# Kernel tuning notes

Measured on AMD Instinct MI355X. Metric: run time of the kernel, lower is better.

Reference implementation:

```python
import jax, jax.numpy as jnp
import numpy as np

# Hardcoded output spatial dims from the original call() (EEG: 62 channels x 375 timesteps)
H, W = 62, 375
N = 16            # batch size
P = H * W         # 23250 patch positions (x_1 dim of cal_val)
KFLAT = 1 * 5 * 25  # flattened kernel size = prod(output_dimension)
F = 64            # number of filters


def setup_inputs() -> dict:
    key = jax.random.key(0)
    k1, k2, k3 = jax.random.split(key, 3)
    x = jax.random.normal(k1, (N, P, KFLAT), dtype=jnp.float32)            # cal_val
    encoding_vector = jax.random.normal(k2, (P, KFLAT), dtype=jnp.float32)
    w = jax.random.normal(k3, (1, 5, 25, F), dtype=jnp.float32) * 0.05      # learned kernel
    return {"x": x, "encoding_vector": encoding_vector, "w": w}


def reference(x, encoding_vector, w):
    n, p, k = x.shape
    f = w.shape[-1]
    # build() flattens each filter: Kernel[j] = w[:, :, :, j].reshape(-1)  -> [F, kflat]
    kernel = jnp.moveaxis(w, 3, 0).reshape(f, k)
    # Original per-filter loop computes sum_k (kernel[f,k] + enc[p,k]) * x[n,p,k]
    # without materializing the tiled [N, P, kflat] kernel tensor:
    # out[f,n,p] = <kernel[f], x[n,p]> + <enc[p], x[n,p]>
    out_fnp = jnp.einsum('fk,npk->fnp', kernel, x) \
        + jnp.einsum('pk,npk->np', encoding_vector, x)[None, :, :]
    # Faithful final reshape of stacked [F, N, P] tensor into [N, F, H, W]
    return out_fnp.reshape(n, f, H, W)
```

## Files before the change

### kernel.cpp

```cpp
#include <hip/hip_runtime.h>


#define P_    23250u
#define K_    125
#define F_    64
#define M_TOT 372000
#define BM    128
#define LDROW 256
#define NBLK  ((M_TOT + BM - 1) / BM)

typedef __bf16 bf16;
typedef __bf16 bf16x4 __attribute__((ext_vector_type(4)));
typedef __bf16 bf16x8 __attribute__((ext_vector_type(8)));
typedef float  f32x4  __attribute__((ext_vector_type(4)));
typedef float  f32x4u __attribute__((ext_vector_type(4), aligned(4)));

__global__ __launch_bounds__(256, 1)
void prep_wfrag(const float* __restrict__ w, bf16* __restrict__ wfrag)
{
    const int tid = threadIdx.x;
    const int f  = ((tid >> 6) << 4) | (tid & 15);
    const int kg = (tid >> 4) & 3;
    #pragma unroll
    for (int ks = 0; ks < 4; ++ks) {
        bf16x8 fr;
        #pragma unroll
        for (int j = 0; j < 8; ++j) {
            const int k = ks * 32 + kg * 8 + j;
            fr[j] = (bf16)((k < K_) ? w[k * F_ + f] : 0.0f);
        }
        *(bf16x8*)(wfrag + tid * 32 + ks * 8) = fr;
    }
}

template<bool USE_WS>
__global__ __launch_bounds__(256, 4)
void eegconv_kernel(const float* __restrict__ x,
                    const float* __restrict__ enc,
                    const float* __restrict__ w,
                    const bf16* __restrict__ wfrag,
                    float* __restrict__ out)
{
    __shared__ bf16  xt[BM * 128];
    __shared__ float srow[BM];

    const int tid  = threadIdx.x;
    const int lane = tid & 63;
    const int wv   = tid >> 6;
    const int fl   = lane & 15;
    const int kg   = lane >> 4;
    const int r0   = blockIdx.x * BM;

    bf16x8 kf[4];
    if (USE_WS) {
        const bf16x8* wf = (const bf16x8*)(wfrag + tid * 32);
        #pragma unroll
        for (int ks = 0; ks < 4; ++ks) kf[ks] = wf[ks];
    } else {
        const int f = wv * 16 + fl;
        #pragma unroll
        for (int ks = 0; ks < 4; ++ks)
            #pragma unroll
            for (int j = 0; j < 8; ++j) {
                const int k = ks * 32 + kg * 8 + j;
                kf[ks][j] = (bf16)((k < K_) ? w[k * F_ + f] : 0.0f);
            }
    }

    {
        const int row = tid >> 1;
        const int t2  = tid & 1;
        int gi = r0 + row;
        const bool rv = gi < M_TOT;
        if (!rv) gi = 0;
        const float* xr = x   + (size_t)gi * K_;
        const float* er = enc + (size_t)((unsigned)gi % P_) * K_;
        char* lbase = (char*)xt + row * LDROW;
        const int sw = (row & 7) << 4;
        float part = 0.0f;

        #pragma unroll
        for (int u = 0; u < 15; ++u) {
            const int c = u * 2 + t2;
            const f32x4 xv = (f32x4)*(const f32x4u*)(xr + c * 4);
            const f32x4 ev = (f32x4)*(const f32x4u*)(er + c * 4);
            part += ev.x * xv.x + ev.y * xv.y + ev.z * xv.z + ev.w * xv.w;
            bf16x4 bv;
            bv[0] = (bf16)xv.x; bv[1] = (bf16)xv.y; bv[2] = (bf16)xv.z; bv[3] = (bf16)xv.w;
            *(bf16x4*)(lbase + ((c * 8) ^ sw)) = bv;
        }
        {
            const int c = 30 + t2;
            f32x4 xv, ev;
            if (t2 == 0) {
                xv = (f32x4)*(const f32x4u*)(xr + 120);
                ev = (f32x4)*(const f32x4u*)(er + 120);
            } else {
                xv = f32x4{xr[124], 0.f, 0.f, 0.f};
                ev = f32x4{er[124], 0.f, 0.f, 0.f};
            }
            part += ev.x * xv.x + ev.y * xv.y + ev.z * xv.z + ev.w * xv.w;
            bf16x4 bv;
            bv[0] = (bf16)xv.x; bv[1] = (bf16)xv.y; bv[2] = (bf16)xv.z; bv[3] = (bf16)xv.w;
            *(bf16x4*)(lbase + ((c * 8) ^ sw)) = bv;
        }
        part += __shfl_xor(part, 1);
        if (t2 == 0) srow[row] = part;
    }
    __syncthreads();

    f32x4 acc[8];
    #pragma unroll
    for (int t = 0; t < 8; ++t) acc[t] = f32x4{0.f, 0.f, 0.f, 0.f};

    #pragma unroll
    for (int t = 0; t < 8; ++t) {
        const int il = t * 16 + fl;
        const char* rbase = (const char*)xt + il * LDROW;
        const int sw = (il & 7) << 4;
        #pragma unroll
        for (int ks = 0; ks < 4; ++ks) {
            const bf16x8 av = *(const bf16x8*)(rbase + ((ks * 64 + kg * 16) ^ sw));
            acc[t] = __builtin_amdgcn_mfma_f32_16x16x32_bf16(av, kf[ks], acc[t], 0, 0, 0);
        }
    }

    const size_t fM = (size_t)(wv * 16 + fl) * (size_t)M_TOT;
    #pragma unroll
    for (int t = 0; t < 8; ++t) {
        const int ib = t * 16 + kg * 4;
        const int i0 = r0 + ib;
        if (i0 < M_TOT) {
            const f32x4 sv = *(const f32x4*)&srow[ib];
            f32x4 v;
            v.x = acc[t][0] + sv.x;
            v.y = acc[t][1] + sv.y;
            v.z = acc[t][2] + sv.z;
            v.w = acc[t][3] + sv.w;
            *(f32x4*)(out + fM + i0) = v;
        }
    }
}

extern "C" void kernel_launch(void* const* d_in, const int* in_sizes, int n_in,
                              void* d_out, int out_size, void* d_ws, size_t ws_size,
                              hipStream_t stream)
{
    const float* x   = (const float*)d_in[0];
    const float* enc = (const float*)d_in[1];
    const float* w   = (const float*)d_in[2];
    float* out = (float*)d_out;

    if (ws_size >= 16384) {
        bf16* wfrag = (bf16*)d_ws;
        prep_wfrag<<<1, 256, 0, stream>>>(w, wfrag);
        eegconv_kernel<true><<<NBLK, 256, 0, stream>>>(x, enc, w, wfrag, out);
    } else {
        eegconv_kernel<false><<<NBLK, 256, 0, stream>>>(x, enc, w, nullptr, out);
    }
}
```

Before: 353.9 us.

## Halve row tile and stage output through LDS for coalesced stores

Cuts the rows per block from 128 to 64 and uses four threads per row for the load and convert stage. Accumulator results now go through a shared-memory transpose (stride 68), so each filter row is written with wider contiguous segments instead of 16-byte scattered stores. Launch bounds rise to 8 blocks per CU to hide latency better, and the non-workspace fallback path is dropped. The cost is extra LDS traffic and barriers, plus a hard dependency on the workspace.

Measured after the change: 355.0 us. Within noise of the previous version (+0.3%).

```diff
diff --git a/kernel.cpp b/kernel.cpp
--- a/kernel.cpp
+++ b/kernel.cpp
@@ -5,9 +5,9 @@
 #define K_    125
 #define F_    64
 #define M_TOT 372000
-#define BM    128
-#define LDROW 256
+#define BM    64
 #define NBLK  ((M_TOT + BM - 1) / BM)
+#define TSTR  68
 
 typedef __bf16 bf16;
 typedef __bf16 bf16x4 __attribute__((ext_vector_type(4)));
@@ -33,16 +33,14 @@
     }
 }
 
-template<bool USE_WS>
-__global__ __launch_bounds__(256, 4)
+__global__ __launch_bounds__(256, 8)
 void eegconv_kernel(const float* __restrict__ x,
                     const float* __restrict__ enc,
-                    const float* __restrict__ w,
                     const bf16* __restrict__ wfrag,
                     float* __restrict__ out)
 {
-    __shared__ bf16  xt[BM * 128];
-    __shared__ float srow[BM];
+    __shared__ __attribute__((aligned(16))) char raw[F_ * TSTR * 4];
+    __shared__ __attribute__((aligned(16))) float srow[BM];
 
     const int tid  = threadIdx.x;
     const int lane = tid & 63;
@@ -52,49 +50,31 @@
     const int r0   = blockIdx.x * BM;
 
     bf16x8 kf[4];
-    if (USE_WS) {
+    {
         const bf16x8* wf = (const bf16x8*)(wfrag + tid * 32);
         #pragma unroll
         for (int ks = 0; ks < 4; ++ks) kf[ks] = wf[ks];
-    } else {
-        const int f = wv * 16 + fl;
-        #pragma unroll
-        for (int ks = 0; ks < 4; ++ks)
-            #pragma unroll
-            for (int j = 0; j < 8; ++j) {
-                const int k = ks * 32 + kg * 8 + j;
-                kf[ks][j] = (bf16)((k < K_) ? w[k * F_ + f] : 0.0f);
-            }
     }
 
+    bf16* xt = (bf16*)raw;
     {
-        const int row = tid >> 1;
-        const int t2  = tid & 1;
+        const int row = tid >> 2;
+        const int t4  = tid & 3;
         int gi = r0 + row;
-        const bool rv = gi < M_TOT;
-        if (!rv) gi = 0;
+        if (gi >= M_TOT) gi = 0;
         const float* xr = x   + (size_t)gi * K_;
         const float* er = enc + (size_t)((unsigned)gi % P_) * K_;
-        char* lbase = (char*)xt + row * LDROW;
+        char* lbase = (char*)xt + row * 256;
         const int sw = (row & 7) << 4;
         float part = 0.0f;
 
         #pragma unroll
-        for (int u = 0; u < 15; ++u) {
-            const int c = u * 2 + t2;
-            const f32x4 xv = (f32x4)*(const f32x4u*)(xr + c * 4);
-            const f32x4 ev = (f32x4)*(const f32x4u*)(er + c * 4);
-            part += ev.x * xv.x + ev.y * xv.y + ev.z * xv.z + ev.w * xv.w;
-            bf16x4 bv;
-            bv[0] = (bf16)xv.x; bv[1] = (bf16)xv.y; bv[2] = (bf16)xv.z; bv[3] = (bf16)xv.w;
-            *(bf16x4*)(lbase + ((c * 8) ^ sw)) = bv;
-        }
-        {
-            const int c = 30 + t2;
+        for (int u = 0; u < 8; ++u) {
+            const int c = u * 4 + t4;
             f32x4 xv, ev;
-            if (t2 == 0) {
-                xv = (f32x4)*(const f32x4u*)(xr + 120);
-                ev = (f32x4)*(const f32x4u*)(er + 120);
+            if (c < 31) {
+                xv = (f32x4)*(const f32x4u*)(xr + c * 4);
+                ev = (f32x4)*(const f32x4u*)(er + c * 4);
             } else {
                 xv = f32x4{xr[124], 0.f, 0.f, 0.f};
                 ev = f32x4{er[124], 0.f, 0.f, 0.f};
@@ -105,18 +85,19 @@
             *(bf16x4*)(lbase + ((c * 8) ^ sw)) = bv;
         }
         part += __shfl_xor(part, 1);
-        if (t2 == 0) srow[row] = part;
+        part += __shfl_xor(part, 2);
+        if (t4 == 0) srow[row] = part;
     }
     __syncthreads();
 
-    f32x4 acc[8];
+    f32x4 acc[4];
     #pragma unroll
-    for (int t = 0; t < 8; ++t) acc[t] = f32x4{0.f, 0.f, 0.f, 0.f};
+    for (int t = 0; t < 4; ++t) acc[t] = f32x4{0.f, 0.f, 0.f, 0.f};
 
     #pragma unroll
-    for (int t = 0; t < 8; ++t) {
+    for (int t = 0; t < 4; ++t) {
         const int il = t * 16 + fl;
-        const char* rbase = (const char*)xt + il * LDROW;
+        const char* rbase = (const char*)xt + il * 256;
         const int sw = (il & 7) << 4;
         #pragma unroll
         for (int ks = 0; ks < 4; ++ks) {
@@ -124,20 +105,37 @@
             acc[t] = __builtin_amdgcn_mfma_f32_16x16x32_bf16(av, kf[ks], acc[t], 0, 0, 0);
         }
     }
+    __syncthreads();
 
-    const size_t fM = (size_t)(wv * 16 + fl) * (size_t)M_TOT;
-    #pragma unroll
-    for (int t = 0; t < 8; ++t) {
-        const int ib = t * 16 + kg * 4;
-        const int i0 = r0 + ib;
-        if (i0 < M_TOT) {
-            const f32x4 sv = *(const f32x4*)&srow[ib];
-            f32x4 v;
-            v.x = acc[t][0] + sv.x;
-            v.y = acc[t][1] + sv.y;
-            v.z = acc[t][2] + sv.z;
-            v.w = acc[t][3] + sv.w;
-            *(f32x4*)(out + fM + i0) = v;
+    float* tr = (float*)raw;
+    {
+        const int f = wv * 16 + fl;
+        #pragma unroll
+        for (int t = 0; t < 4; ++t) {
+            const int i0 = t * 16 + kg * 4;
+            *(f32x4*)(tr + f * TSTR + i0) = acc[t];
+        }
+    }
+    __syncthreads();
+
+    {
+        const int m8 = tid & 7;
+        const int fg = tid >> 3;
+        #pragma unroll
+        for (int p = 0; p < 2; ++p) {
+            const int f = p * 32 + fg;
+            const float* src = tr + f * TSTR;
+            const size_t ob = (size_t)f * M_TOT + r0;
+            #pragma unroll
+            for (int h = 0; h < 2; ++h) {
+                const int ii = h * 32 + m8 * 4;
+                if (r0 + ii < M_TOT) {
+                    f32x4 v  = *(const f32x4*)(src + ii);
+                    const f32x4 sv = *(const f32x4*)(srow + ii);
+                    v.x += sv.x; v.y += sv.y; v.z += sv.z; v.w += sv.w;
+                    *(f32x4*)(out + ob + ii) = v;
+                }
+            }
         }
     }
 }
@@ -150,12 +148,7 @@
     const float* enc = (const float*)d_in[1];
     const float* w   = (const float*)d_in[2];
     float* out = (float*)d_out;
-
-    if (ws_size >= 16384) {
-        bf16* wfrag = (bf16*)d_ws;
-        prep_wfrag<<<1, 256, 0, stream>>>(w, wfrag);
-        eegconv_kernel<true><<<NBLK, 256, 0, stream>>>(x, enc, w, wfrag, out);
-    } else {
-        eegconv_kernel<false><<<NBLK, 256, 0, stream>>>(x, enc, w, nullptr, out);
-    }
+    bf16* wfrag = (bf16*)d_ws;
+    prep_wfrag<<<1, 256, 0, stream>>>(w, wfrag);
+    eegconv_kernel<<<NBLK, 256, 0, stream>>>(x, enc, wfrag, out);
 }
```
